# Performance work log

Hardware: AMD Instinct MI355X
Metric: run time of the kernel (lower is better)

The kernel has to match this reference:

```python
import jax, jax.numpy as jnp
import numpy as np

VOCAB = 30001  # vocab_size + 1
EMB = 64
CHAR = 50
RNN = 128
TAGS = 9
B, T = 256, 512
D_IN = EMB + CHAR  # 114


def lstm_scan(x, Wx, Wh, b):
    # x: [T, B, D]; Keras LSTM gate order i, f, g(c), o; sigmoid/tanh activations.
    Bsz = x.shape[1]
    H = Wh.shape[0]
    def step(carry, xt):
        h, c = carry
        z = xt @ Wx + h @ Wh + b  # [B, 4H]
        i, f, g, o = jnp.split(z, 4, axis=-1)
        c = jax.nn.sigmoid(f) * c + jax.nn.sigmoid(i) * jnp.tanh(g)
        h = jax.nn.sigmoid(o) * jnp.tanh(c)
        return (h, c), h
    init = (jnp.zeros((Bsz, H), x.dtype), jnp.zeros((Bsz, H), x.dtype))
    _, hs = jax.lax.scan(step, init, x)
    return hs  # [T, B, H]


def crf_log_likelihood(logits, labels, lengths, trans):
    # logits: [B,T,K]; labels: [B,T] int; lengths: [B] int; trans: [K,K]
    Bsz, Tlen, K = logits.shape
    mask = (jnp.arange(Tlen)[None, :] < lengths[:, None]).astype(logits.dtype)  # [B,T]
    # gold path score: unary + pairwise transition terms
    unary = jnp.take_along_axis(logits, labels[..., None], axis=-1)[..., 0]  # [B,T]
    unary_score = jnp.sum(unary * mask, axis=1)
    binary = trans[labels[:, :-1], labels[:, 1:]]  # [B,T-1]
    binary_score = jnp.sum(binary * mask[:, 1:], axis=1)
    seq_score = unary_score + binary_score
    # forward algorithm (log-domain scan over time)
    logits_t = jnp.transpose(logits, (1, 0, 2))  # [T,B,K]
    mask_t = jnp.transpose(mask[:, 1:])          # [T-1,B]
    def step(alpha, inp):
        logit_t, m = inp
        new = jax.nn.logsumexp(alpha[:, :, None] + trans[None], axis=1) + logit_t
        alpha = jnp.where(m[:, None] > 0, new, alpha)
        return alpha, None
    alpha, _ = jax.lax.scan(step, logits_t[0], (logits_t[1:], mask_t))
    log_norm = jax.nn.logsumexp(alpha, axis=1)
    log_norm = jnp.where(lengths > 0, log_norm, jnp.zeros_like(log_norm))
    return seq_score - log_norm


def setup_inputs() -> dict:
    key = jax.random.key(0)
    ks = jax.random.split(key, 12)
    inputs = jax.random.randint(ks[0], (B, T), 0, 30000, dtype=jnp.int32)
    char_embeddings = jax.random.normal(ks[1], (B, T, CHAR), dtype=jnp.float32)
    labels = jax.random.randint(ks[2], (B, T), 0, TAGS, dtype=jnp.int32)
    E = 0.1 * jax.random.normal(ks[3], (VOCAB, EMB), dtype=jnp.float32)
    s_in = 1.0 / np.sqrt(D_IN)
    s_h = 1.0 / np.sqrt(RNN)
    Wx_f = s_in * jax.random.normal(ks[4], (D_IN, 4 * RNN), dtype=jnp.float32)
    Wh_f = s_h * jax.random.normal(ks[5], (RNN, 4 * RNN), dtype=jnp.float32)
    b_f = jnp.zeros((4 * RNN,), jnp.float32)
    Wx_b = s_in * jax.random.normal(ks[6], (D_IN, 4 * RNN), dtype=jnp.float32)
    Wh_b = s_h * jax.random.normal(ks[7], (RNN, 4 * RNN), dtype=jnp.float32)
    b_b = jnp.zeros((4 * RNN,), jnp.float32)
    Wd = (1.0 / np.sqrt(2 * RNN)) * jax.random.normal(ks[8], (2 * RNN, TAGS), dtype=jnp.float32)
    bd = jnp.zeros((TAGS,), jnp.float32)
    transition = jax.random.uniform(ks[9], (TAGS, TAGS), dtype=jnp.float32)
    return {"inputs": inputs, "char_embeddings": char_embeddings, "labels": labels,
            "E": E, "Wx_f": Wx_f, "Wh_f": Wh_f, "b_f": b_f,
            "Wx_b": Wx_b, "Wh_b": Wh_b, "b_b": b_b,
            "Wd": Wd, "bd": bd, "transition": transition}


def reference(inputs, char_embeddings, labels, E, Wx_f, Wh_f, b_f, Wx_b, Wh_b, b_b, Wd, bd, transition):
    emb = E[inputs]                                      # [B,T,64]
    x = jnp.concatenate([emb, char_embeddings], axis=2)  # [B,T,114]
    xt = jnp.transpose(x, (1, 0, 2))                     # [T,B,114]
    h_f = lstm_scan(xt, Wx_f, Wh_f, b_f)                 # [T,B,128]
    h_b = lstm_scan(xt[::-1], Wx_b, Wh_b, b_b)[::-1]     # [T,B,128]
    out = jnp.concatenate([h_f, h_b], axis=-1)           # [T,B,256]
    logits = jnp.transpose(out, (1, 0, 2)) @ Wd + bd     # [B,T,9]
    lengths = jnp.sum((labels != 0).astype(jnp.int32), axis=1)
    log_likelihood = crf_log_likelihood(logits, labels, lengths, transition)
    return log_likelihood, transition
```

## Files before the change

### kernel.cpp

```cpp
#include <hip/hip_runtime.h>

#define BB   256
#define TT   512
#define EMBD 64
#define CHARD 50
#define DIN  114
#define RNN  128
#define NG   512
#define TAGS 9

typedef __bf16 bf16x8 __attribute__((ext_vector_type(8)));
typedef float  f32x4  __attribute__((ext_vector_type(4)));
typedef unsigned int u32x2 __attribute__((ext_vector_type(2)));

static __device__ __forceinline__ unsigned short f2bf(float f) {
  unsigned int u = __float_as_uint(f);
  unsigned int r = (u + 0x7FFFu + ((u >> 16) & 1u)) >> 16;
  return (unsigned short)r;
}
static __device__ __forceinline__ void gl_lds16(const void* g, void* l) {
  __builtin_amdgcn_global_load_lds(
      (const __attribute__((address_space(1))) unsigned int*)g,
      (__attribute__((address_space(3))) unsigned int*)l, 16, 0, 0);
}

__global__ void k_build_x(const int* __restrict__ inp, const float* __restrict__ ch,
                          const float* __restrict__ E, unsigned short* __restrict__ x) {
  int idx = blockIdx.x * 256 + threadIdx.x;
  int k   = idx & 127;
  int row = idx >> 7;
  float v;
  if (k < EMBD)      v = E[inp[row] * EMBD + k];
  else if (k < DIN)  v = ch[row * CHARD + (k - EMBD)];
  else               v = 0.f;
  x[idx] = f2bf(v);
}

__global__ void k_prep_w(const float* __restrict__ Wx_f, const float* __restrict__ Wh_f,
                         const float* __restrict__ Wx_b, const float* __restrict__ Wh_b,
                         const float* __restrict__ Wd,
                         unsigned short* __restrict__ WxT, unsigned short* __restrict__ WhT,
                         unsigned short* __restrict__ WdT) {
  if (blockIdx.x == 512) {
    for (int i = threadIdx.x; i < 16 * 256; i += 256) {
      int n = i >> 8, k = i & 255;
      WdT[i] = (n < TAGS) ? f2bf(Wd[k * TAGS + n]) : (unsigned short)0;
    }
    return;
  }
  int idx = blockIdx.x * 256 + threadIdx.x;
  int dir = idx >> 16;
  int rem = idx & 65535;
  int n   = rem >> 7;
  int kk  = rem & 127;
  const float* Wx = dir ? Wx_b : Wx_f;
  const float* Wh = dir ? Wh_b : Wh_f;
  WxT[idx] = (kk < DIN) ? f2bf(Wx[kk * NG + n]) : (unsigned short)0;
  WhT[idx] = f2bf(Wh[kk * NG + n]);
}

__global__ void k_lengths(const int* __restrict__ labels, int* __restrict__ lengths) {
  int b = blockIdx.x, lane = threadIdx.x;
  int cnt = 0;
  for (int t = lane; t < TT; t += 64) cnt += (labels[b * TT + t] != 0);
  for (int o = 32; o > 0; o >>= 1) cnt += __shfl_down(cnt, o);
  if (lane == 0) lengths[b] = cnt;
}

__global__ __launch_bounds__(512, 2) void k_fused(
    const unsigned short* __restrict__ x,
    const unsigned short* __restrict__ WxT,
    const unsigned short* __restrict__ WhT,
    const float* __restrict__ b_f, const float* __restrict__ b_b,
    const unsigned short* __restrict__ zcons, unsigned short* __restrict__ zprod,
    unsigned short* __restrict__ hseq, float* __restrict__ cbuf,
    int lstm_n, int s0, int s1, int first, int zs0, int znsteps)
{
  __shared__ __align__(16) char LDS[32768];
  const int tid = threadIdx.x, w = tid >> 6, l = tid & 63;
  const int lq = l & 15, lg = l >> 4;

  if ((int)blockIdx.x < lstm_n) {
    const int wg = blockIdx.x, dir = wg >> 5, rg = wg & 31, b0 = rg * 8;
    const unsigned short* WhD = WhT + dir * (NG * 128);
    unsigned short* hout = hseq + (size_t)dir * ((size_t)BB * TT * 128);
    char* ring = LDS;

    bf16x8 wh[4][4];
    #pragma unroll
    for (int g = 0; g < 4; ++g)
      #pragma unroll
      for (int kt = 0; kt < 4; ++kt)
        wh[g][kt] = *reinterpret_cast<const bf16x8*>(
            WhD + (g * RNN + w * 16 + lq) * 128 + kt * 32 + lg * 8);

    const int row7 = l & 7;
    int ro[4];
    #pragma unroll
    for (int kt = 0; kt < 4; ++kt)
      ro[kt] = (row7 * 16 + (((kt * 4) + lg) ^ row7)) * 16;

    int wo[2], rowr[2];
    #pragma unroll
    for (int rr = 0; rr < 2; ++rr) {
      rowr[rr] = (lg & 1) * 4 + (lg >> 1) * 2 + rr;
      int unit = rowr[rr] * 16 + ((w * 2 + (lq >> 3)) ^ rowr[rr]);
      wo[rr] = unit * 16 + (lq & 7) * 2;
    }
    const int hidden = w * 16 + lq;

    if (tid < 128) {
      int row = tid >> 4, h16 = tid & 15;
      int unit = row * 16 + (h16 ^ row);
      if (first) {
        *reinterpret_cast<f32x4*>(ring + 7 * 2048 + unit * 16) = f32x4{0.f, 0.f, 0.f, 0.f};
      } else {
        int tprev = dir ? (TT - s0) : (s0 - 1);
        bf16x8 v = *reinterpret_cast<const bf16x8*>(
            hout + ((size_t)(b0 + row) * TT + tprev) * 128 + h16 * 8);
        *reinterpret_cast<bf16x8*>(ring + 7 * 2048 + unit * 16) = v;
      }
    }
    float c[2];
    #pragma unroll
    for (int rr = 0; rr < 2; ++rr)
      c[rr] = first ? 0.f : cbuf[(size_t)(dir * BB + b0 + rowr[rr]) * RNN + hidden];
    __syncthreads();

    const unsigned short* zQ = zcons +
        (size_t)(((dir * 32 + rg) * 8 + w) * 2 + (lg & 1)) * 256 + lq * 4;
    u32x2 zA[4], zB[4];
    if (lg < 2) {
      #pragma unroll
      for (int g = 0; g < 4; ++g) zA[g] = *reinterpret_cast<const u32x2*>(zQ + g * 64);
      const unsigned short* zp1 = zQ + (size_t)((s0 + 1 < s1) ? 1 : 0) * 262144;
      #pragma unroll
      for (int g = 0; g < 4; ++g) zB[g] = *reinterpret_cast<const u32x2*>(zp1 + g * 64);
    }

    auto gather = [&](int sp) {
      int h16 = tid & 15, tc = (tid >> 4) & 3, row = tid >> 6;
      int ss = sp + tc, t = dir ? (TT - 1 - ss) : ss;
      bf16x8 v = *reinterpret_cast<const bf16x8*>(
          ring + (ss & 7) * 2048 + (row * 16 + (h16 ^ row)) * 16);
      *reinterpret_cast<bf16x8*>(hout + ((size_t)(b0 + row) * TT + t) * 128 + h16 * 8) = v;
    };

    for (int s = s0; s < s1; ++s) {
      f32x4 acc[4];
      #pragma unroll
      for (int g = 0; g < 4; ++g) {
        unsigned int lo = zA[g][0], hi = zA[g][1];
        f32x4 zv = f32x4{__uint_as_float(lo << 16), __uint_as_float(lo & 0xffff0000u),
                         __uint_as_float(hi << 16), __uint_as_float(hi & 0xffff0000u)};
        acc[g] = (lg < 2) ? zv : f32x4{0.f, 0.f, 0.f, 0.f};
      }
      {
        #pragma unroll
        for (int g = 0; g < 4; ++g) zA[g] = zB[g];
        int sn = (s + 2 < s1) ? (s + 2) : (s1 - 1);
        if (lg < 2) {
          const unsigned short* zp = zQ + (size_t)(sn - s0) * 262144;
          #pragma unroll
          for (int g = 0; g < 4; ++g) zB[g] = *reinterpret_cast<const u32x2*>(zp + g * 64);
        }
      }

      const char* rb = ring + ((s - 1) & 7) * 2048;
      bf16x8 hf[4];
      #pragma unroll
      for (int kt = 0; kt < 4; ++kt)
        hf[kt] = *reinterpret_cast<const bf16x8*>(rb + ro[kt]);
      #pragma unroll
      for (int kt = 0; kt < 4; ++kt)
        #pragma unroll
        for (int g = 0; g < 4; ++g)
          acc[g] = __builtin_amdgcn_mfma_f32_16x16x32_bf16(hf[kt], wh[g][kt], acc[g], 0, 0, 0);

      if ((s & 3) == 0 && s > s0) gather(s - 4);

      float sw_[4][2];
      #pragma unroll
      for (int g = 0; g < 4; ++g)
        #pragma unroll
        for (int rr = 0; rr < 2; ++rr) {
          float d = acc[g][2 + rr], sv = acc[g][2 + rr];
          asm volatile("v_permlane32_swap_b32 %0, %1" : "+v"(d), "+v"(sv));
          sw_[g][rr] = d;
        }

      char* wslot = ring + (s & 7) * 2048;
      #pragma unroll
      for (int rr = 0; rr < 2; ++rr) {
        float zi = (lg < 2) ? acc[0][rr] : sw_[0][rr];
        float zf = (lg < 2) ? acc[1][rr] : sw_[1][rr];
        float zg = (lg < 2) ? acc[2][rr] : sw_[2][rr];
        float zo = (lg < 2) ? acc[3][rr] : sw_[3][rr];
        zi = fminf(20.f, fmaxf(-20.f, zi));
        zf = fminf(20.f, fmaxf(-20.f, zf));
        zg = fminf(20.f, fmaxf(-20.f, zg));
        zo = fminf(20.f, fmaxf(-20.f, zo));
        float ei = __expf(-zi), ef = __expf(-zf), eo = __expf(-zo);
        float g2 = __expf(2.f * zg);
        float P   = (1.f + ei) * (g2 + 1.f);
        float efp = 1.f + ef;
        float cn  = (c[rr] * P + efp * (g2 - 1.f)) * __builtin_amdgcn_rcpf(efp * P);
        c[rr] = cn;
        float cc = fminf(20.f, fmaxf(-20.f, cn));
        float ec = __expf(2.f * cc);
        float hn = (ec - 1.f) * __builtin_amdgcn_rcpf((1.f + eo) * (ec + 1.f));
        *reinterpret_cast<unsigned short*>(wslot + wo[rr]) = f2bf(hn);
      }
      __builtin_amdgcn_sched_barrier(0);
      asm volatile("s_waitcnt lgkmcnt(0)" ::: "memory");
      __builtin_amdgcn_s_barrier();
      __builtin_amdgcn_sched_barrier(0);
    }

    gather(s1 - 4);
    #pragma unroll
    for (int rr = 0; rr < 2; ++rr)
      cbuf[(size_t)(dir * BB + b0 + rowr[rr]) * RNN + hidden] = c[rr];
  } else {
    if (znsteps <= 0) return;
    const int TCHN = znsteps >> 4;
    const int zb = blockIdx.x - lstm_n;
    const int per = 16 * TCHN;
    const int dir = zb / per;
    const int rem = zb % per;
    const int rg2 = rem / TCHN, tch = rem % TCHN;
    const int b0p = rg2 * 16;
    const int sb  = zs0 + tch * 16;

    const unsigned short* WxD = WxT + dir * (NG * 128);
    const float* bias = dir ? b_b : b_f;
    unsigned short* xr = (unsigned short*)LDS;

    bf16x8 wx[4][4];
    float  bs[4];
    #pragma unroll
    for (int g = 0; g < 4; ++g) {
      int n = g * RNN + w * 16 + lq;
      bs[g] = bias[n];
      #pragma unroll
      for (int kt = 0; kt < 4; ++kt)
        wx[g][kt] = *reinterpret_cast<const bf16x8*>(WxD + n * 128 + kt * 32 + lg * 8);
    }

    auto stage = [&](int ci) {
      int buf = ci & 1;
      #pragma unroll
      for (int jj = 0; jj < 2; ++jj) {
        int idx = w * 2 + jj, sc = idx >> 2, kt = idx & 3;
        int s = sb + ci * 4 + sc;
        int t = dir ? (TT - 1 - s) : s;
        gl_lds16(x + ((size_t)(b0p + lq) * TT + t) * 128 + kt * 32 + lg * 8,
                 xr + buf * 8192 + sc * 2048 + kt * 512);
      }
    };

    stage(0);
    for (int ci = 0; ci < 4; ++ci) {
      __syncthreads();
      if (ci < 3) stage(ci + 1);
      int buf = ci & 1;
      #pragma unroll
      for (int sc = 0; sc < 4; ++sc) {
        int s = sb + ci * 4 + sc;
        bf16x8 xf[4];
        #pragma unroll
        for (int kt = 0; kt < 4; ++kt)
          xf[kt] = *reinterpret_cast<const bf16x8*>(xr + buf * 8192 + sc * 2048 + kt * 512 + l * 8);
        f32x4 acc[4];
        #pragma unroll
        for (int g = 0; g < 4; ++g) acc[g] = f32x4{bs[g], bs[g], bs[g], bs[g]};
        #pragma unroll
        for (int kt = 0; kt < 4; ++kt)
          #pragma unroll
          for (int g = 0; g < 4; ++g)
            acc[g] = __builtin_amdgcn_mfma_f32_16x16x32_bf16(xf[kt], wx[g][kt], acc[g], 0, 0, 0);
        unsigned short* zp = zprod + (size_t)(s - zs0) * 262144 +
            (size_t)(((dir * 32 + rg2 * 2 + (lg >> 1)) * 8 + w) * 2 + (lg & 1)) * 256 + lq * 4;
        #pragma unroll
        for (int g = 0; g < 4; ++g) {
          ushort4 v;
          v.x = f2bf(acc[g][0]); v.y = f2bf(acc[g][1]);
          v.z = f2bf(acc[g][2]); v.w = f2bf(acc[g][3]);
          *reinterpret_cast<ushort4*>(zp + g * 64) = v;
        }
      }
    }
  }
}

__global__ __launch_bounds__(256) void k_logits(const unsigned short* __restrict__ hseq,
                                                const unsigned short* __restrict__ WdT,
                                                const float* __restrict__ bd,
                                                float* __restrict__ logits,
                                                float* __restrict__ euk) {
  __shared__ __align__(16) unsigned short xt[2][16384];
  const int tid = threadIdx.x, wv = tid >> 6, l = tid & 63;
  const int lq = l & 15, lg = l >> 4;
  const size_t HS = (size_t)BB * TT * 128;

  bf16x8 wb[8];
  #pragma unroll
  for (int kt = 0; kt < 8; ++kt)
    wb[kt] = *reinterpret_cast<const bf16x8*>(WdT + lq * 256 + kt * 32 + lg * 8);
  float bdv = (lq < TAGS) ? bd[lq] : 0.f;

  auto stage = [&](int it, int buf) {
    int bt0 = blockIdx.x * 256 + it * 64;
    #pragma unroll
    for (int i = 0; i < 8; ++i) {
      int v = tid + i * 256;
      int g = v ^ ((v >> 5) & 7);
      int row = g >> 5, cu = g & 31;
      const unsigned short* src = (cu < 16)
          ? hseq + (size_t)(bt0 + row) * 128 + cu * 8
          : hseq + HS + (size_t)(bt0 + row) * 128 + (cu - 16) * 8;
      gl_lds16(src, &xt[buf][(i * 256 + wv * 64) * 8]);
    }
  };

  stage(0, 0);
  for (int it = 0; it < 4; ++it) {
    __syncthreads();
    if (it < 3) stage(it + 1, (it + 1) & 1);
    int buf = it & 1;
    int bt0 = blockIdx.x * 256 + it * 64;
    int r0 = wv * 16;
    bf16x8 af[8];
    #pragma unroll
    for (int kt = 0; kt < 8; ++kt) {
      int u = (r0 + lq) * 32 + kt * 4 + lg;
      af[kt] = *reinterpret_cast<const bf16x8*>(&xt[buf][(u ^ ((u >> 5) & 7)) * 8]);
    }
    f32x4 acc = f32x4{bdv, bdv, bdv, bdv};
    #pragma unroll
    for (int kt = 0; kt < 8; ++kt)
      acc = __builtin_amdgcn_mfma_f32_16x16x32_bf16(af[kt], wb[kt], acc, 0, 0, 0);
    float mr[4];
    #pragma unroll
    for (int r = 0; r < 4; ++r) {
      float v = (lq < TAGS) ? acc[r] : -1e30f;
      #pragma unroll
      for (int o = 1; o < 16; o <<= 1) v = fmaxf(v, __shfl_xor(v, o, 16));
      mr[r] = v;
    }
    #pragma unroll
    for (int r = 0; r < 4; ++r) {
      int rowi = bt0 + r0 + lg * 4 + r;
      if (lq < TAGS) logits[(size_t)rowi * TAGS + lq] = acc[r];
      if (lq < 12) {
        float val = (lq < TAGS) ? __expf(acc[r] - mr[r]) : ((lq == TAGS) ? mr[r] : 0.f);
        euk[(size_t)rowi * 12 + lq] = val;
      }
    }
  }
}

__global__ void k_score(const float* __restrict__ logits, const int* __restrict__ labels,
                        const int* __restrict__ lengths, const float* __restrict__ trans,
                        float* __restrict__ scbuf) {
  int b = blockIdx.x, lane = threadIdx.x;
  int len = lengths[b];
  const float* lg = logits + (size_t)b * TT * TAGS;
  const int*   lab = labels + b * TT;
  float sc = 0.f;
  for (int t = lane; t < TT; t += 64) {
    if (t < len) {
      sc += lg[t * TAGS + lab[t]];
      if (t >= 1) sc += trans[lab[t - 1] * TAGS + lab[t]];
    }
  }
  for (int o = 32; o > 0; o >>= 1) sc += __shfl_down(sc, o);
  if (lane == 0) scbuf[b] = sc;
}

__global__ __launch_bounds__(256, 1) void k_crf2(const float* __restrict__ euk,
                                                 const float* __restrict__ scbuf,
                                                 const int* __restrict__ lengths,
                                                 const float* __restrict__ trans,
                                                 float* __restrict__ out) {
  const int wv = threadIdx.x >> 6, lane = threadIdx.x & 63;
  const int b = blockIdx.x * 4 + wv;
  const float* ep = euk + (size_t)b * TT * 12;
  const int len = lengths[b];
  const int lim = (len < TT) ? len : TT;

  float Et[81];
  #pragma unroll
  for (int i = 0; i < 81; ++i) Et[i] = __expf(trans[i]);

  float P[81];
  float Ks = 0.f;
  int   E2 = 0;

  const int t0 = 1 + lane * 8;
  auto rec = [&](int t) { int tl = (t < TT) ? t : (TT - 1); return ep + (size_t)tl * 12; };

  const float* p0 = rec(t0);
  float4 A0 = *(const float4*)p0, A1 = *(const float4*)(p0 + 4), A2 = *(const float4*)(p0 + 8);
  const float* p1 = rec(t0 + 1);
  float4 B0 = *(const float4*)p1, B1 = *(const float4*)(p1 + 4), B2 = *(const float4*)(p1 + 8);

  {
    float eu[9] = {A0.x, A0.y, A0.z, A0.w, A1.x, A1.y, A1.z, A1.w, A2.x};
    bool upd = t0 < lim;
    #pragma unroll
    for (int i = 0; i < 9; ++i)
      #pragma unroll
      for (int j = 0; j < 9; ++j)
        P[i * 9 + j] = upd ? Et[i * 9 + j] * eu[j] : ((i == j) ? 1.f : 0.f);
    Ks += upd ? A2.y : 0.f;
    A0 = B0; A1 = B1; A2 = B2;
    const float* pn = rec(t0 + 2);
    B0 = *(const float4*)pn; B1 = *(const float4*)(pn + 4); B2 = *(const float4*)(pn + 8);
  }

  for (int s = 1; s < 8; ++s) {
    float eu[9] = {A0.x, A0.y, A0.z, A0.w, A1.x, A1.y, A1.z, A1.w, A2.x};
    float mt = A2.y;
    bool upd = (t0 + s) < lim;
    A0 = B0; A1 = B1; A2 = B2;
    const float* pn = rec(t0 + s + 2);
    B0 = *(const float4*)pn; B1 = *(const float4*)(pn + 4); B2 = *(const float4*)(pn + 8);
    #pragma unroll
    for (int i = 0; i < 9; ++i) {
      float tmp[9];
      #pragma unroll
      for (int j = 0; j < 9; ++j) {
        float a = P[i * 9 + 0] * Et[0 * 9 + j];
        #pragma unroll
        for (int k = 1; k < 9; ++k) a = fmaf(P[i * 9 + k], Et[k * 9 + j], a);
        tmp[j] = a * eu[j];
      }
      #pragma unroll
      for (int j = 0; j < 9; ++j) P[i * 9 + j] = upd ? tmp[j] : P[i * 9 + j];
    }
    Ks += upd ? mt : 0.f;
  }

  {
    float m = P[0];
    #pragma unroll
    for (int e = 1; e < 81; ++e) m = fmaxf(m, P[e]);
    int ex; frexpf(m, &ex);
    #pragma unroll
    for (int e = 0; e < 81; ++e) P[e] = ldexpf(P[e], -ex);
    E2 += ex;
  }

  for (int d = 0; d < 6; ++d) {
    int msk = 1 << d;
    float Q[81];
    #pragma unroll
    for (int e = 0; e < 81; ++e) Q[e] = __shfl_xor(P[e], msk);
    int   E2p = __shfl_xor(E2, msk);
    float Ksp = __shfl_xor(Ks, msk);
    bool late = (lane & msk) != 0;
    #pragma unroll
    for (int e = 0; e < 81; ++e) {
      float a = P[e], q = Q[e];
      P[e] = late ? q : a;
      Q[e] = late ? a : q;
    }
    #pragma unroll
    for (int i = 0; i < 9; ++i) {
      float tmp[9];
      #pragma unroll
      for (int j = 0; j < 9; ++j) {
        float a = P[i * 9 + 0] * Q[0 * 9 + j];
        #pragma unroll
        for (int k = 1; k < 9; ++k) a = fmaf(P[i * 9 + k], Q[k * 9 + j], a);
        tmp[j] = a;
      }
      #pragma unroll
      for (int j = 0; j < 9; ++j) P[i * 9 + j] = tmp[j];
    }
    E2 += E2p; Ks += Ksp;
    float m = P[0];
    #pragma unroll
    for (int e = 1; e < 81; ++e) m = fmaxf(m, P[e]);
    int ex; frexpf(m, &ex);
    #pragma unroll
    for (int e = 0; e < 81; ++e) P[e] = ldexpf(P[e], -ex);
    E2 += ex;
  }

  float4 z0 = *(const float4*)ep, z1 = *(const float4*)(ep + 4), z2 = *(const float4*)(ep + 8);
  float eu0[9] = {z0.x, z0.y, z0.z, z0.w, z1.x, z1.y, z1.z, z1.w, z2.x};
  float alpha[9];
  #pragma unroll
  for (int j = 0; j < 9; ++j) {
    float a = eu0[0] * P[0 * 9 + j];
    #pragma unroll
    for (int i = 1; i < 9; ++i) a = fmaf(eu0[i], P[i * 9 + j], a);
    alpha[j] = a;
  }
  float S = ((alpha[0] + alpha[1]) + (alpha[2] + alpha[3])) +
            ((alpha[4] + alpha[5]) + (alpha[6] + alpha[7])) + alpha[8];
  float ln = logf(S) + (float)E2 * 0.69314718056f + Ks + z2.y;
  if (lane == 0) out[b] = (len > 0) ? (scbuf[b] - ln) : 0.f;
}

__global__ void k_copy_trans(const float* __restrict__ trans, float* __restrict__ out) {
  int i = threadIdx.x;
  if (i < TAGS * TAGS) out[BB + i] = trans[i];
}

extern "C" void kernel_launch(void* const* d_in, const int* in_sizes, int n_in,
                              void* d_out, int out_size, void* d_ws, size_t ws_size,
                              hipStream_t stream) {
  const int*   inp    = (const int*)d_in[0];
  const float* ch     = (const float*)d_in[1];
  const int*   labels = (const int*)d_in[2];
  const float* E      = (const float*)d_in[3];
  const float* Wx_f   = (const float*)d_in[4];
  const float* Wh_f   = (const float*)d_in[5];
  const float* b_f    = (const float*)d_in[6];
  const float* Wx_b   = (const float*)d_in[7];
  const float* Wh_b   = (const float*)d_in[8];
  const float* b_b    = (const float*)d_in[9];
  const float* Wd     = (const float*)d_in[10];
  const float* bd     = (const float*)d_in[11];
  const float* trans  = (const float*)d_in[12];
  float* out = (float*)d_out;

  unsigned short* x    = (unsigned short*)d_ws;
  unsigned short* hseq = x + (size_t)BB * TT * 128;
  unsigned short* WxT  = hseq + (size_t)2 * BB * TT * 128;
  unsigned short* WhT  = WxT + 2 * NG * 128;
  unsigned short* WdT  = WhT + 2 * NG * 128;
  float* logits        = (float*)(WdT + 16 * 256);
  float* euk           = logits + (size_t)BB * TT * TAGS;
  float* cbuf          = euk + (size_t)BB * TT * 12;
  float* scbuf         = cbuf + (size_t)2 * BB * RNN;
  int*   lengths       = (int*)(scbuf + BB);
  unsigned short* zbuf = (unsigned short*)(lengths + 256);

  const size_t zoff = (size_t)((char*)zbuf - (char*)d_ws);
  int NP = 4;
  const int cands[4] = {4, 8, 16, 32};
  for (int i = 0; i < 4; ++i) {
    NP = cands[i];
    if (zoff + 2ull * (size_t)(TT / NP) * 524288ull <= ws_size) break;
  }
  const int L = TT / NP;
  const size_t zsl = (size_t)L * 262144;

  k_build_x<<<(BB * TT * 128) / 256, 256, 0, stream>>>(inp, ch, E, x);
  k_prep_w<<<513, 256, 0, stream>>>(Wx_f, Wh_f, Wx_b, Wh_b, Wd, WxT, WhT, WdT);
  k_lengths<<<BB, 64, 0, stream>>>(labels, lengths);

  k_fused<<<2 * 16 * (L / 16), 512, 0, stream>>>(x, WxT, WhT, b_f, b_b,
                                                 zbuf, zbuf, hseq, cbuf,
                                                 0, 0, 0, 1, 0, L);
  for (int p = 0; p < NP; ++p) {
    int nz = (p + 1 < NP) ? 2 * 16 * (L / 16) : 0;
    k_fused<<<64 + nz, 512, 0, stream>>>(
        x, WxT, WhT, b_f, b_b,
        zbuf + (size_t)(p & 1) * zsl,
        zbuf + (size_t)((p + 1) & 1) * zsl,
        hseq, cbuf,
        64, p * L, (p + 1) * L, (p == 0) ? 1 : 0, (p + 1) * L, nz ? L : 0);
  }

  k_logits<<<(BB * TT) / 256, 256, 0, stream>>>(hseq, WdT, bd, logits, euk);
  k_score<<<BB, 64, 0, stream>>>(logits, labels, lengths, trans, scbuf);
  k_crf2<<<BB / 4, 256, 0, stream>>>(euk, scbuf, lengths, trans, out);
  k_copy_trans<<<1, 128, 0, stream>>>(trans, out);
}
```

Measured before the change: 605.6 us.

## Split LSTM recurrence over 128 workgroups of 4 rows, fold log2e into weights

The recurrent LSTM phase now uses 128 workgroups, each owning 4 batch rows instead of 8. Each lane therefore handles one gate element per step instead of two, which shortens the serial per-step critical path at the cost of doubling the workgroups that hold the recurrent weights. The z-buffer layout and LDS ring slots are resized to match. Wx, Wh and the bias are pre-scaled by log2(e) so the gate activations can use exp2 directly, which changes the bf16 rounding of the weights slightly.

```diff
diff --git a/kernel.cpp b/kernel.cpp
--- a/kernel.cpp
+++ b/kernel.cpp
@@ -8,6 +8,7 @@
 #define RNN  128
 #define NG   512
 #define TAGS 9
+#define LOG2E 1.4426950408889634f
 
 typedef __bf16 bf16x8 __attribute__((ext_vector_type(8)));
 typedef float  f32x4  __attribute__((ext_vector_type(4)));
@@ -55,8 +56,8 @@
   int kk  = rem & 127;
   const float* Wx = dir ? Wx_b : Wx_f;
   const float* Wh = dir ? Wh_b : Wh_f;
-  WxT[idx] = (kk < DIN) ? f2bf(Wx[kk * NG + n]) : (unsigned short)0;
-  WhT[idx] = f2bf(Wh[kk * NG + n]);
+  WxT[idx] = (kk < DIN) ? f2bf(LOG2E * Wx[kk * NG + n]) : (unsigned short)0;
+  WhT[idx] = f2bf(LOG2E * Wh[kk * NG + n]);
 }
 
 __global__ void k_lengths(const int* __restrict__ labels, int* __restrict__ lengths) {
@@ -81,7 +82,7 @@
   const int lq = l & 15, lg = l >> 4;
 
   if ((int)blockIdx.x < lstm_n) {
-    const int wg = blockIdx.x, dir = wg >> 5, rg = wg & 31, b0 = rg * 8;
+    const int wg = blockIdx.x, dir = wg >> 6, rg = wg & 63, b0 = rg * 4;
     const unsigned short* WhD = WhT + dir * (NG * 128);
     unsigned short* hout = hseq + (size_t)dir * ((size_t)BB * TT * 128);
     char* ring = LDS;
@@ -94,56 +95,50 @@
         wh[g][kt] = *reinterpret_cast<const bf16x8*>(
             WhD + (g * RNN + w * 16 + lq) * 128 + kt * 32 + lg * 8);
 
-    const int row7 = l & 7;
+    const int rq = lq & 3;
     int ro[4];
     #pragma unroll
     for (int kt = 0; kt < 4; ++kt)
-      ro[kt] = (row7 * 16 + (((kt * 4) + lg) ^ row7)) * 16;
-
-    int wo[2], rowr[2];
-    #pragma unroll
-    for (int rr = 0; rr < 2; ++rr) {
-      rowr[rr] = (lg & 1) * 4 + (lg >> 1) * 2 + rr;
-      int unit = rowr[rr] * 16 + ((w * 2 + (lq >> 3)) ^ rowr[rr]);
-      wo[rr] = unit * 16 + (lq & 7) * 2;
-    }
+      ro[kt] = (rq * 16 + (((kt * 4) + lg) ^ rq)) * 16;
+
     const int hidden = w * 16 + lq;
-
-    if (tid < 128) {
+    const int wo = (lg * 16 + ((w * 2 + (lq >> 3)) ^ lg)) * 16 + (lq & 7) * 2;
+
+    if (tid < 64) {
       int row = tid >> 4, h16 = tid & 15;
       int unit = row * 16 + (h16 ^ row);
       if (first) {
-        *reinterpret_cast<f32x4*>(ring + 7 * 2048 + unit * 16) = f32x4{0.f, 0.f, 0.f, 0.f};
+        *reinterpret_cast<f32x4*>(ring + 7 * 1024 + unit * 16) = f32x4{0.f, 0.f, 0.f, 0.f};
       } else {
         int tprev = dir ? (TT - s0) : (s0 - 1);
         bf16x8 v = *reinterpret_cast<const bf16x8*>(
             hout + ((size_t)(b0 + row) * TT + tprev) * 128 + h16 * 8);
-        *reinterpret_cast<bf16x8*>(ring + 7 * 2048 + unit * 16) = v;
-      }
-    }
-    float c[2];
-    #pragma unroll
-    for (int rr = 0; rr < 2; ++rr)
-      c[rr] = first ? 0.f : cbuf[(size_t)(dir * BB + b0 + rowr[rr]) * RNN + hidden];
+        *reinterpret_cast<bf16x8*>(ring + 7 * 1024 + unit * 16) = v;
+      }
+    }
+    float c1 = first ? 0.f : cbuf[(size_t)(dir * BB + b0 + lg) * RNN + hidden];
     __syncthreads();
 
-    const unsigned short* zQ = zcons +
-        (size_t)(((dir * 32 + rg) * 8 + w) * 2 + (lg & 1)) * 256 + lq * 4;
+    const unsigned short* zQ = zcons + (size_t)((dir * 64 + rg) * 8 + w) * 256;
     u32x2 zA[4], zB[4];
-    if (lg < 2) {
-      #pragma unroll
-      for (int g = 0; g < 4; ++g) zA[g] = *reinterpret_cast<const u32x2*>(zQ + g * 64);
+    if (lg == 0) {
+      #pragma unroll
+      for (int g = 0; g < 4; ++g)
+        zA[g] = *reinterpret_cast<const u32x2*>(zQ + g * 64 + lq * 4);
       const unsigned short* zp1 = zQ + (size_t)((s0 + 1 < s1) ? 1 : 0) * 262144;
       #pragma unroll
-      for (int g = 0; g < 4; ++g) zB[g] = *reinterpret_cast<const u32x2*>(zp1 + g * 64);
+      for (int g = 0; g < 4; ++g)
+        zB[g] = *reinterpret_cast<const u32x2*>(zp1 + g * 64 + lq * 4);
     }
 
     auto gather = [&](int sp) {
-      int h16 = tid & 15, tc = (tid >> 4) & 3, row = tid >> 6;
-      int ss = sp + tc, t = dir ? (TT - 1 - ss) : ss;
-      bf16x8 v = *reinterpret_cast<const bf16x8*>(
-          ring + (ss & 7) * 2048 + (row * 16 + (h16 ^ row)) * 16);
-      *reinterpret_cast<bf16x8*>(hout + ((size_t)(b0 + row) * TT + t) * 128 + h16 * 8) = v;
+      if (tid < 256) {
+        int h16 = tid & 15, tc = (tid >> 4) & 3, row = tid >> 6;
+        int ss = sp + tc, t = dir ? (TT - 1 - ss) : ss;
+        bf16x8 v = *reinterpret_cast<const bf16x8*>(
+            ring + (ss & 7) * 1024 + (row * 16 + (h16 ^ row)) * 16);
+        *reinterpret_cast<bf16x8*>(hout + ((size_t)(b0 + row) * TT + t) * 128 + h16 * 8) = v;
+      }
     };
 
     for (int s = s0; s < s1; ++s) {
@@ -153,20 +148,21 @@
         unsigned int lo = zA[g][0], hi = zA[g][1];
         f32x4 zv = f32x4{__uint_as_float(lo << 16), __uint_as_float(lo & 0xffff0000u),
                          __uint_as_float(hi << 16), __uint_as_float(hi & 0xffff0000u)};
-        acc[g] = (lg < 2) ? zv : f32x4{0.f, 0.f, 0.f, 0.f};
+        acc[g] = (lg == 0) ? zv : f32x4{0.f, 0.f, 0.f, 0.f};
       }
       {
         #pragma unroll
         for (int g = 0; g < 4; ++g) zA[g] = zB[g];
         int sn = (s + 2 < s1) ? (s + 2) : (s1 - 1);
-        if (lg < 2) {
+        if (lg == 0) {
           const unsigned short* zp = zQ + (size_t)(sn - s0) * 262144;
           #pragma unroll
-          for (int g = 0; g < 4; ++g) zB[g] = *reinterpret_cast<const u32x2*>(zp + g * 64);
+          for (int g = 0; g < 4; ++g)
+            zB[g] = *reinterpret_cast<const u32x2*>(zp + g * 64 + lq * 4);
         }
       }
 
-      const char* rb = ring + ((s - 1) & 7) * 2048;
+      const char* rb = ring + ((s - 1) & 7) * 1024;
       bf16x8 hf[4];
       #pragma unroll
       for (int kt = 0; kt < 4; ++kt)
@@ -179,38 +175,36 @@
 
       if ((s & 3) == 0 && s > s0) gather(s - 4);
 
-      float sw_[4][2];
-      #pragma unroll
-      for (int g = 0; g < 4; ++g)
-        #pragma unroll
-        for (int rr = 0; rr < 2; ++rr) {
-          float d = acc[g][2 + rr], sv = acc[g][2 + rr];
-          asm volatile("v_permlane32_swap_b32 %0, %1" : "+v"(d), "+v"(sv));
-          sw_[g][rr] = d;
-        }
-
-      char* wslot = ring + (s & 7) * 2048;
-      #pragma unroll
-      for (int rr = 0; rr < 2; ++rr) {
-        float zi = (lg < 2) ? acc[0][rr] : sw_[0][rr];
-        float zf = (lg < 2) ? acc[1][rr] : sw_[1][rr];
-        float zg = (lg < 2) ? acc[2][rr] : sw_[2][rr];
-        float zo = (lg < 2) ? acc[3][rr] : sw_[3][rr];
-        zi = fminf(20.f, fmaxf(-20.f, zi));
-        zf = fminf(20.f, fmaxf(-20.f, zf));
-        zg = fminf(20.f, fmaxf(-20.f, zg));
-        zo = fminf(20.f, fmaxf(-20.f, zo));
-        float ei = __expf(-zi), ef = __expf(-zf), eo = __expf(-zo);
-        float g2 = __expf(2.f * zg);
-        float P   = (1.f + ei) * (g2 + 1.f);
-        float efp = 1.f + ef;
-        float cn  = (c[rr] * P + efp * (g2 - 1.f)) * __builtin_amdgcn_rcpf(efp * P);
-        c[rr] = cn;
-        float cc = fminf(20.f, fmaxf(-20.f, cn));
-        float ec = __expf(2.f * cc);
-        float hn = (ec - 1.f) * __builtin_amdgcn_rcpf((1.f + eo) * (ec + 1.f));
-        *reinterpret_cast<unsigned short*>(wslot + wo[rr]) = f2bf(hn);
-      }
+      float zg4[4];
+      #pragma unroll
+      for (int g = 0; g < 4; ++g) {
+        float a0 = acc[g][0];
+        float s1v = acc[g][1], s1d = acc[g][1];
+        asm volatile("v_permlane16_swap_b32 %0, %1" : "+v"(s1v), "+v"(s1d));
+        float s2v = acc[g][2], s2d = acc[g][2];
+        asm volatile("v_permlane32_swap_b32 %0, %1" : "+v"(s2v), "+v"(s2d));
+        float s3v = acc[g][3], s3d = acc[g][3];
+        asm volatile("v_permlane16_swap_b32 %0, %1" : "+v"(s3v), "+v"(s3d));
+        float s3e = s3v, s3f = s3v;
+        asm volatile("v_permlane32_swap_b32 %0, %1" : "+v"(s3e), "+v"(s3f));
+        zg4[g] = (lg == 0) ? a0 : (lg == 1) ? s1v : (lg == 2) ? s2v : s3e;
+      }
+
+      float zi = fminf(28.8539f, fmaxf(-28.8539f, zg4[0]));
+      float zf = fminf(28.8539f, fmaxf(-28.8539f, zg4[1]));
+      float zg = fminf(28.8539f, fmaxf(-28.8539f, zg4[2]));
+      float zo = fminf(28.8539f, fmaxf(-28.8539f, zg4[3]));
+      float ei = exp2f(-zi), ef = exp2f(-zf), eo = exp2f(-zo);
+      float g2 = exp2f(2.f * zg);
+      float P   = (1.f + ei) * (g2 + 1.f);
+      float efp = 1.f + ef;
+      float cn  = (c1 * P + efp * (g2 - 1.f)) * __builtin_amdgcn_rcpf(efp * P);
+      c1 = cn;
+      float tcv = fminf(57.7078f, fmaxf(-57.7078f, cn * (2.f * LOG2E)));
+      float ec = exp2f(tcv);
+      float hn = (ec - 1.f) * __builtin_amdgcn_rcpf((1.f + eo) * (ec + 1.f));
+      *reinterpret_cast<unsigned short*>(ring + (s & 7) * 1024 + wo) = f2bf(hn);
+
       __builtin_amdgcn_sched_barrier(0);
       asm volatile("s_waitcnt lgkmcnt(0)" ::: "memory");
       __builtin_amdgcn_s_barrier();
@@ -218,9 +212,7 @@
     }
 
     gather(s1 - 4);
-    #pragma unroll
-    for (int rr = 0; rr < 2; ++rr)
-      cbuf[(size_t)(dir * BB + b0 + rowr[rr]) * RNN + hidden] = c[rr];
+    cbuf[(size_t)(dir * BB + b0 + lg) * RNN + hidden] = c1;
   } else {
     if (znsteps <= 0) return;
     const int TCHN = znsteps >> 4;
@@ -241,7 +233,7 @@
     #pragma unroll
     for (int g = 0; g < 4; ++g) {
       int n = g * RNN + w * 16 + lq;
-      bs[g] = bias[n];
+      bs[g] = LOG2E * bias[n];
       #pragma unroll
       for (int kt = 0; kt < 4; ++kt)
         wx[g][kt] = *reinterpret_cast<const bf16x8*>(WxD + n * 128 + kt * 32 + lg * 8);
@@ -280,7 +272,7 @@
           for (int g = 0; g < 4; ++g)
             acc[g] = __builtin_amdgcn_mfma_f32_16x16x32_bf16(xf[kt], wx[g][kt], acc[g], 0, 0, 0);
         unsigned short* zp = zprod + (size_t)(s - zs0) * 262144 +
-            (size_t)(((dir * 32 + rg2 * 2 + (lg >> 1)) * 8 + w) * 2 + (lg & 1)) * 256 + lq * 4;
+            (size_t)((dir * 64 + rg2 * 4 + lg) * 8 + w) * 256 + lq * 4;
         #pragma unroll
         for (int g = 0; g < 4; ++g) {
           ushort4 v;
@@ -559,12 +551,12 @@
                                                  0, 0, 0, 1, 0, L);
   for (int p = 0; p < NP; ++p) {
     int nz = (p + 1 < NP) ? 2 * 16 * (L / 16) : 0;
-    k_fused<<<64 + nz, 512, 0, stream>>>(
+    k_fused<<<128 + nz, 512, 0, stream>>>(
         x, WxT, WhT, b_f, b_b,
         zbuf + (size_t)(p & 1) * zsl,
         zbuf + (size_t)((p + 1) & 1) * zsl,
         hseq, cbuf,
-        64, p * L, (p + 1) * L, (p == 0) ? 1 : 0, (p + 1) * L, nz ? L : 0);
+        128, p * L, (p + 1) * L, (p == 0) ? 1 : 0, (p + 1) * L, nz ? L : 0);
   }
 
   k_logits<<<(BB * TT) / 256, 256, 0, stream>>>(hseq, WdT, bd, logits, euk);
```

Measured after the change: 643.2 us. +6.2%, slower.

## Prescale LSTM weights by log2e, split MFMA accumulators, raise recurrent priority

Applied to the files above, without the earlier changes.

Folds log2(e) into the Wx, Wh and bias values at preprocessing so the recurrent gate math can call exp2 directly, removing the per-element multiply that __expf adds. The 16 dependent MFMAs per step are split into four independent accumulator chains that are summed afterwards, which shortens the serial MFMA dependency on the critical recurrence. It also raises wave priority for the LSTM blocks and changes launch bounds from 2 to 1 blocks per CU, which allows more registers but may reduce co-residency with the producer blocks. Rounding the prescaled weights to bf16 shifts numerics slightly.

```diff
diff --git a/kernel.cpp b/kernel.cpp
--- a/kernel.cpp
+++ b/kernel.cpp
@@ -8,6 +8,7 @@
 #define RNN  128
 #define NG   512
 #define TAGS 9
+#define LOG2E 1.4426950408889634f
 
 typedef __bf16 bf16x8 __attribute__((ext_vector_type(8)));
 typedef float  f32x4  __attribute__((ext_vector_type(4)));
@@ -55,8 +56,8 @@
   int kk  = rem & 127;
   const float* Wx = dir ? Wx_b : Wx_f;
   const float* Wh = dir ? Wh_b : Wh_f;
-  WxT[idx] = (kk < DIN) ? f2bf(Wx[kk * NG + n]) : (unsigned short)0;
-  WhT[idx] = f2bf(Wh[kk * NG + n]);
+  WxT[idx] = (kk < DIN) ? f2bf(LOG2E * Wx[kk * NG + n]) : (unsigned short)0;
+  WhT[idx] = f2bf(LOG2E * Wh[kk * NG + n]);
 }
 
 __global__ void k_lengths(const int* __restrict__ labels, int* __restrict__ lengths) {
@@ -67,7 +68,7 @@
   if (lane == 0) lengths[b] = cnt;
 }
 
-__global__ __launch_bounds__(512, 2) void k_fused(
+__global__ __launch_bounds__(512, 1) void k_fused(
     const unsigned short* __restrict__ x,
     const unsigned short* __restrict__ WxT,
     const unsigned short* __restrict__ WhT,
@@ -81,6 +82,7 @@
   const int lq = l & 15, lg = l >> 4;
 
   if ((int)blockIdx.x < lstm_n) {
+    __builtin_amdgcn_s_setprio(1);
     const int wg = blockIdx.x, dir = wg >> 5, rg = wg & 31, b0 = rg * 8;
     const unsigned short* WhD = WhT + dir * (NG * 128);
     unsigned short* hout = hseq + (size_t)dir * ((size_t)BB * TT * 128);
@@ -147,13 +149,16 @@
     };
 
     for (int s = s0; s < s1; ++s) {
-      f32x4 acc[4];
+      f32x4 p0[4], p1[4], p2[4], p3[4];
       #pragma unroll
       for (int g = 0; g < 4; ++g) {
         unsigned int lo = zA[g][0], hi = zA[g][1];
         f32x4 zv = f32x4{__uint_as_float(lo << 16), __uint_as_float(lo & 0xffff0000u),
                          __uint_as_float(hi << 16), __uint_as_float(hi & 0xffff0000u)};
-        acc[g] = (lg < 2) ? zv : f32x4{0.f, 0.f, 0.f, 0.f};
+        p0[g] = (lg < 2) ? zv : f32x4{0.f, 0.f, 0.f, 0.f};
+        p1[g] = f32x4{0.f, 0.f, 0.f, 0.f};
+        p2[g] = f32x4{0.f, 0.f, 0.f, 0.f};
+        p3[g] = f32x4{0.f, 0.f, 0.f, 0.f};
       }
       {
         #pragma unroll
@@ -172,12 +177,18 @@
       for (int kt = 0; kt < 4; ++kt)
         hf[kt] = *reinterpret_cast<const bf16x8*>(rb + ro[kt]);
       #pragma unroll
-      for (int kt = 0; kt < 4; ++kt)
-        #pragma unroll
-        for (int g = 0; g < 4; ++g)
-          acc[g] = __builtin_amdgcn_mfma_f32_16x16x32_bf16(hf[kt], wh[g][kt], acc[g], 0, 0, 0);
+      for (int g = 0; g < 4; ++g) {
+        p0[g] = __builtin_amdgcn_mfma_f32_16x16x32_bf16(hf[0], wh[g][0], p0[g], 0, 0, 0);
+        p1[g] = __builtin_amdgcn_mfma_f32_16x16x32_bf16(hf[1], wh[g][1], p1[g], 0, 0, 0);
+        p2[g] = __builtin_amdgcn_mfma_f32_16x16x32_bf16(hf[2], wh[g][2], p2[g], 0, 0, 0);
+        p3[g] = __builtin_amdgcn_mfma_f32_16x16x32_bf16(hf[3], wh[g][3], p3[g], 0, 0, 0);
+      }
 
       if ((s & 3) == 0 && s > s0) gather(s - 4);
+
+      f32x4 acc[4];
+      #pragma unroll
+      for (int g = 0; g < 4; ++g) acc[g] = (p0[g] + p1[g]) + (p2[g] + p3[g]);
 
       float sw_[4][2];
       #pragma unroll
@@ -196,18 +207,18 @@
         float zf = (lg < 2) ? acc[1][rr] : sw_[1][rr];
         float zg = (lg < 2) ? acc[2][rr] : sw_[2][rr];
         float zo = (lg < 2) ? acc[3][rr] : sw_[3][rr];
-        zi = fminf(20.f, fmaxf(-20.f, zi));
-        zf = fminf(20.f, fmaxf(-20.f, zf));
-        zg = fminf(20.f, fmaxf(-20.f, zg));
-        zo = fminf(20.f, fmaxf(-20.f, zo));
-        float ei = __expf(-zi), ef = __expf(-zf), eo = __expf(-zo);
-        float g2 = __expf(2.f * zg);
+        zi = fminf(28.8539f, fmaxf(-28.8539f, zi));
+        zf = fminf(28.8539f, fmaxf(-28.8539f, zf));
+        zg = fminf(28.8539f, fmaxf(-28.8539f, zg));
+        zo = fminf(28.8539f, fmaxf(-28.8539f, zo));
+        float ei = exp2f(-zi), ef = exp2f(-zf), eo = exp2f(-zo);
+        float g2 = exp2f(2.f * zg);
         float P   = (1.f + ei) * (g2 + 1.f);
         float efp = 1.f + ef;
         float cn  = (c[rr] * P + efp * (g2 - 1.f)) * __builtin_amdgcn_rcpf(efp * P);
         c[rr] = cn;
-        float cc = fminf(20.f, fmaxf(-20.f, cn));
-        float ec = __expf(2.f * cc);
+        float tcv = fminf(57.7078f, fmaxf(-57.7078f, cn * (2.f * LOG2E)));
+        float ec = exp2f(tcv);
         float hn = (ec - 1.f) * __builtin_amdgcn_rcpf((1.f + eo) * (ec + 1.f));
         *reinterpret_cast<unsigned short*>(wslot + wo[rr]) = f2bf(hn);
       }
@@ -241,7 +252,7 @@
     #pragma unroll
     for (int g = 0; g < 4; ++g) {
       int n = g * RNN + w * 16 + lq;
-      bs[g] = bias[n];
+      bs[g] = LOG2E * bias[n];
       #pragma unroll
       for (int kt = 0; kt < 4; ++kt)
         wx[g][kt] = *reinterpret_cast<const bf16x8*>(WxD + n * 128 + kt * 32 + lg * 8);
```

Result: slower. 758.3 us (+25.2%).

## Store input-projection Z in fp32 and split recurrent MFMA accumulation chains

Applied to the files above, without the earlier changes.

The precomputed x·Wx gate projections are now stored and loaded as fp32 instead of bf16. This removes the per-element bf16 pack and unpack work, at the cost of doubling the z buffer traffic and workspace size, which may force more pipeline phases (NP). The recurrent MFMA loop now uses two independent accumulator chains (a01, a23) that are summed afterwards, to shorten the dependent MFMA latency chain on the serial critical path. The sched_barriers around the step barrier are also removed, letting the compiler reorder across them.

```diff
diff --git a/kernel.cpp b/kernel.cpp
--- a/kernel.cpp
+++ b/kernel.cpp
@@ -11,7 +11,6 @@
 
 typedef __bf16 bf16x8 __attribute__((ext_vector_type(8)));
 typedef float  f32x4  __attribute__((ext_vector_type(4)));
-typedef unsigned int u32x2 __attribute__((ext_vector_type(2)));
 
 static __device__ __forceinline__ unsigned short f2bf(float f) {
   unsigned int u = __float_as_uint(f);
@@ -72,7 +71,7 @@
     const unsigned short* __restrict__ WxT,
     const unsigned short* __restrict__ WhT,
     const float* __restrict__ b_f, const float* __restrict__ b_b,
-    const unsigned short* __restrict__ zcons, unsigned short* __restrict__ zprod,
+    const float* __restrict__ zcons, float* __restrict__ zprod,
     unsigned short* __restrict__ hseq, float* __restrict__ cbuf,
     int lstm_n, int s0, int s1, int first, int zs0, int znsteps)
 {
@@ -127,15 +126,15 @@
       c[rr] = first ? 0.f : cbuf[(size_t)(dir * BB + b0 + rowr[rr]) * RNN + hidden];
     __syncthreads();
 
-    const unsigned short* zQ = zcons +
+    const float* zQ = zcons +
         (size_t)(((dir * 32 + rg) * 8 + w) * 2 + (lg & 1)) * 256 + lq * 4;
-    u32x2 zA[4], zB[4];
+    f32x4 zA[4], zB[4];
     if (lg < 2) {
       #pragma unroll
-      for (int g = 0; g < 4; ++g) zA[g] = *reinterpret_cast<const u32x2*>(zQ + g * 64);
-      const unsigned short* zp1 = zQ + (size_t)((s0 + 1 < s1) ? 1 : 0) * 262144;
-      #pragma unroll
-      for (int g = 0; g < 4; ++g) zB[g] = *reinterpret_cast<const u32x2*>(zp1 + g * 64);
+      for (int g = 0; g < 4; ++g) zA[g] = *reinterpret_cast<const f32x4*>(zQ + g * 64);
+      const float* zp1 = zQ + (size_t)((s0 + 1 < s1) ? 1 : 0) * 262144;
+      #pragma unroll
+      for (int g = 0; g < 4; ++g) zB[g] = *reinterpret_cast<const f32x4*>(zp1 + g * 64);
     }
 
     auto gather = [&](int sp) {
@@ -147,22 +146,20 @@
     };
 
     for (int s = s0; s < s1; ++s) {
-      f32x4 acc[4];
+      f32x4 a01[4], a23[4];
       #pragma unroll
       for (int g = 0; g < 4; ++g) {
-        unsigned int lo = zA[g][0], hi = zA[g][1];
-        f32x4 zv = f32x4{__uint_as_float(lo << 16), __uint_as_float(lo & 0xffff0000u),
-                         __uint_as_float(hi << 16), __uint_as_float(hi & 0xffff0000u)};
-        acc[g] = (lg < 2) ? zv : f32x4{0.f, 0.f, 0.f, 0.f};
+        a01[g] = (lg < 2) ? zA[g] : f32x4{0.f, 0.f, 0.f, 0.f};
+        a23[g] = f32x4{0.f, 0.f, 0.f, 0.f};
       }
       {
         #pragma unroll
         for (int g = 0; g < 4; ++g) zA[g] = zB[g];
         int sn = (s + 2 < s1) ? (s + 2) : (s1 - 1);
         if (lg < 2) {
-          const unsigned short* zp = zQ + (size_t)(sn - s0) * 262144;
+          const float* zp = zQ + (size_t)(sn - s0) * 262144;
           #pragma unroll
-          for (int g = 0; g < 4; ++g) zB[g] = *reinterpret_cast<const u32x2*>(zp + g * 64);
+          for (int g = 0; g < 4; ++g) zB[g] = *reinterpret_cast<const f32x4*>(zp + g * 64);
         }
       }
 
@@ -172,12 +169,18 @@
       for (int kt = 0; kt < 4; ++kt)
         hf[kt] = *reinterpret_cast<const bf16x8*>(rb + ro[kt]);
       #pragma unroll
-      for (int kt = 0; kt < 4; ++kt)
-        #pragma unroll
-        for (int g = 0; g < 4; ++g)
-          acc[g] = __builtin_amdgcn_mfma_f32_16x16x32_bf16(hf[kt], wh[g][kt], acc[g], 0, 0, 0);
+      for (int g = 0; g < 4; ++g) {
+        a01[g] = __builtin_amdgcn_mfma_f32_16x16x32_bf16(hf[0], wh[g][0], a01[g], 0, 0, 0);
+        a23[g] = __builtin_amdgcn_mfma_f32_16x16x32_bf16(hf[2], wh[g][2], a23[g], 0, 0, 0);
+        a01[g] = __builtin_amdgcn_mfma_f32_16x16x32_bf16(hf[1], wh[g][1], a01[g], 0, 0, 0);
+        a23[g] = __builtin_amdgcn_mfma_f32_16x16x32_bf16(hf[3], wh[g][3], a23[g], 0, 0, 0);
+      }
 
       if ((s & 3) == 0 && s > s0) gather(s - 4);
+
+      f32x4 acc[4];
+      #pragma unroll
+      for (int g = 0; g < 4; ++g) acc[g] = a01[g] + a23[g];
 
       float sw_[4][2];
       #pragma unroll
@@ -211,10 +214,8 @@
         float hn = (ec - 1.f) * __builtin_amdgcn_rcpf((1.f + eo) * (ec + 1.f));
         *reinterpret_cast<unsigned short*>(wslot + wo[rr]) = f2bf(hn);
       }
-      __builtin_amdgcn_sched_barrier(0);
       asm volatile("s_waitcnt lgkmcnt(0)" ::: "memory");
       __builtin_amdgcn_s_barrier();
-      __builtin_amdgcn_sched_barrier(0);
     }
 
     gather(s1 - 4);
@@ -279,15 +280,11 @@
           #pragma unroll
           for (int g = 0; g < 4; ++g)
             acc[g] = __builtin_amdgcn_mfma_f32_16x16x32_bf16(xf[kt], wx[g][kt], acc[g], 0, 0, 0);
-        unsigned short* zp = zprod + (size_t)(s - zs0) * 262144 +
+        float* zp = zprod + (size_t)(s - zs0) * 262144 +
             (size_t)(((dir * 32 + rg2 * 2 + (lg >> 1)) * 8 + w) * 2 + (lg & 1)) * 256 + lq * 4;
         #pragma unroll
-        for (int g = 0; g < 4; ++g) {
-          ushort4 v;
-          v.x = f2bf(acc[g][0]); v.y = f2bf(acc[g][1]);
-          v.z = f2bf(acc[g][2]); v.w = f2bf(acc[g][3]);
-          *reinterpret_cast<ushort4*>(zp + g * 64) = v;
-        }
+        for (int g = 0; g < 4; ++g)
+          *reinterpret_cast<f32x4*>(zp + g * 64) = acc[g];
       }
     }
   }
@@ -538,14 +535,14 @@
   float* cbuf          = euk + (size_t)BB * TT * 12;
   float* scbuf         = cbuf + (size_t)2 * BB * RNN;
   int*   lengths       = (int*)(scbuf + BB);
-  unsigned short* zbuf = (unsigned short*)(lengths + 256);
+  float* zbuf          = (float*)(lengths + 256);
 
   const size_t zoff = (size_t)((char*)zbuf - (char*)d_ws);
   int NP = 4;
   const int cands[4] = {4, 8, 16, 32};
   for (int i = 0; i < 4; ++i) {
     NP = cands[i];
-    if (zoff + 2ull * (size_t)(TT / NP) * 524288ull <= ws_size) break;
+    if (zoff + 2ull * (size_t)(TT / NP) * 1048576ull <= ws_size) break;
   }
   const int L = TT / NP;
   const size_t zsl = (size_t)L * 262144;
```

After: 649.7 us. 1.07x slower.
